# Kernel tuning notes

Measured on AMD Instinct MI355X. Metric: run time of the kernel, lower is better.

## Reference

```python
import jax, jax.numpy as jnp
import numpy as np

N_QUESTION = 10000
B, S = 256, 500
Q_DIM = 128
QA_DIM = 128
M = 64            # memory_size
KEY_DIM = 128
VAL_DIM = 256


def setup_inputs() -> dict:
    key = jax.random.key(0)
    ks = jax.random.split(key, 10)
    q_data = jax.random.randint(ks[0], (B, S), 0, N_QUESTION + 1)
    qa_data = jax.random.randint(ks[1], (B, S), 0, 2 * N_QUESTION + 1)
    # embedding tables with padding_idx=0 zeroed
    q_embed_w = jax.random.normal(ks[2], (N_QUESTION + 1, Q_DIM), jnp.float32) * 0.05
    q_embed_w = q_embed_w.at[0].set(0.0)
    qa_embed_w = jax.random.normal(ks[3], (2 * N_QUESTION + 1, QA_DIM), jnp.float32) * 0.05
    qa_embed_w = qa_embed_w.at[0].set(0.0)
    key_mem = jax.random.normal(ks[4], (M, KEY_DIM), jnp.float32) * (2.0 / KEY_DIM) ** 0.5
    init_value_mem = jax.random.normal(ks[5], (M, VAL_DIM), jnp.float32) * (2.0 / VAL_DIM) ** 0.5
    erase_W = jax.random.normal(ks[6], (QA_DIM, VAL_DIM), jnp.float32) * (2.0 / QA_DIM) ** 0.5
    erase_b = jnp.zeros((VAL_DIM,), jnp.float32)
    add_W = jax.random.normal(ks[7], (QA_DIM, VAL_DIM), jnp.float32) * (2.0 / QA_DIM) ** 0.5
    add_b = jnp.zeros((VAL_DIM,), jnp.float32)
    return {
        "q_data": q_data, "qa_data": qa_data,
        "q_embed_w": q_embed_w, "qa_embed_w": qa_embed_w,
        "key_mem": key_mem, "init_value_mem": init_value_mem,
        "erase_W": erase_W, "erase_b": erase_b,
        "add_W": add_W, "add_b": add_b,
    }


def reference(q_data, qa_data, q_embed_w, qa_embed_w, key_mem, init_value_mem,
              erase_W, erase_b, add_W, add_b):
    q_emb = q_embed_w[q_data]     # [B,S,Qd]
    qa_emb = qa_embed_w[qa_data]  # [B,S,QAd]
    write_mask = (q_data >= 1).astype(jnp.float32)  # [B,S]

    Mv0 = jnp.broadcast_to(init_value_mem[None], (q_data.shape[0], M, VAL_DIM))

    def step(Mv, xs):
        q_t, qa_t, m_t = xs  # [B,Qd], [B,QAd], [B]
        # attention over memory slots
        w = jax.nn.softmax(q_t @ key_mem.T, axis=-1)           # [B,M]
        read = jnp.einsum('bm,bmd->bd', w, Mv)                 # [B,D]
        erase = jax.nn.sigmoid(qa_t @ erase_W + erase_b)       # [B,D]
        add = jnp.tanh(qa_t @ add_W + add_b)                   # [B,D]
        new_Mv = Mv * (1.0 - w[:, :, None] * erase[:, None, :]) \
                 + w[:, :, None] * add[:, None, :]
        Mv = jnp.where(m_t[:, None, None] > 0, new_Mv, Mv)
        return Mv, read

    xs = (jnp.swapaxes(q_emb, 0, 1), jnp.swapaxes(qa_emb, 0, 1),
          jnp.swapaxes(write_mask, 0, 1))
    _, reads = jax.lax.scan(step, Mv0, xs)        # reads: [S,B,D]
    reads = jnp.swapaxes(reads, 0, 1)             # [B,S,D]
    # shift right by one timestep, zero-pad first step
    out = jnp.concatenate([jnp.zeros_like(reads[:, :1]), reads[:, :-1]], axis=1)
    return out
```

## Files before the change

### kernel.cpp

```cpp
#include <hip/hip_runtime.h>
#include <math.h>

#define B_     256
#define S_     500
#define QD_    128
#define M_     64
#define VD_    256
#define CH_    16
#define NQ_    10000
#define NQA_   20000
#define WROWS  (NQ_ + 1)
#define EAROWS (NQA_ + 1)

typedef unsigned int u32;

__device__ __forceinline__ void gload_lds16(const float* g, float* l)
{
    __builtin_amdgcn_global_load_lds(
        (const __attribute__((address_space(1))) u32*)(const void*)g,
        (__attribute__((address_space(3))) u32*)(void*)l, 16, 0, 0);
}

__device__ __forceinline__ float qadd1(float x)
{
    int r = __builtin_amdgcn_mov_dpp(__float_as_int(x), 0xB1, 0xF, 0xF, true);
    return x + __int_as_float(r);
}
__device__ __forceinline__ float qadd2(float x)
{
    int r = __builtin_amdgcn_mov_dpp(__float_as_int(x), 0x4E, 0xF, 0xF, true);
    return x + __int_as_float(r);
}

__global__ void kT_kernel(const float* __restrict__ key_mem, float4* __restrict__ kTq)
{
    int i = blockIdx.x * 256 + threadIdx.x;
    if (i < 32 * 64) {
        int m  = i & 63;
        int k4 = i >> 6;
        kTq[i] = *reinterpret_cast<const float4*>(&key_mem[m * QD_ + k4 * 4]);
    }
}

__global__ __launch_bounds__(256) void wtab_kernel(
    const float*  __restrict__ q_embed_w,
    const float4* __restrict__ kTq,
    float*        __restrict__ wtab)
{
    __shared__ float4 q4[16][32];

    const int tid = threadIdx.x;
    const int r0  = blockIdx.x * 16;

    for (int i = tid; i < 512; i += 256) {
        int row = i >> 5, k4 = i & 31;
        int r   = r0 + row; if (r > NQ_) r = NQ_;
        q4[row][k4] = *reinterpret_cast<const float4*>(
            &q_embed_w[(size_t)r * QD_ + k4 * 4]);
    }
    __syncthreads();

    const int wave = tid >> 6, lane = tid & 63;
    const int rr = wave * 4;

    float s0 = 0.f, s1 = 0.f, s2 = 0.f, s3 = 0.f;
    for (int k4 = 0; k4 < 32; ++k4) {
        float4 kv = kTq[k4 * 64 + lane];
        float4 a0 = q4[rr + 0][k4];
        float4 a1 = q4[rr + 1][k4];
        float4 a2 = q4[rr + 2][k4];
        float4 a3 = q4[rr + 3][k4];
        s0 = fmaf(a0.x, kv.x, s0); s0 = fmaf(a0.y, kv.y, s0);
        s0 = fmaf(a0.z, kv.z, s0); s0 = fmaf(a0.w, kv.w, s0);
        s1 = fmaf(a1.x, kv.x, s1); s1 = fmaf(a1.y, kv.y, s1);
        s1 = fmaf(a1.z, kv.z, s1); s1 = fmaf(a1.w, kv.w, s1);
        s2 = fmaf(a2.x, kv.x, s2); s2 = fmaf(a2.y, kv.y, s2);
        s2 = fmaf(a2.z, kv.z, s2); s2 = fmaf(a2.w, kv.w, s2);
        s3 = fmaf(a3.x, kv.x, s3); s3 = fmaf(a3.y, kv.y, s3);
        s3 = fmaf(a3.z, kv.z, s3); s3 = fmaf(a3.w, kv.w, s3);
    }

    float s[4] = { s0, s1, s2, s3 };
    #pragma unroll
    for (int j = 0; j < 4; ++j) {
        float mx = s[j];
        #pragma unroll
        for (int off = 32; off; off >>= 1) mx = fmaxf(mx, __shfl_xor(mx, off));
        float e = __expf(s[j] - mx);
        float sum = e;
        #pragma unroll
        for (int off = 32; off; off >>= 1) sum += __shfl_xor(sum, off);
        if (r0 + rr + j < WROWS)
            wtab[(size_t)(r0 + rr + j) * 64 + lane] = e / sum;
    }
}

__global__ __launch_bounds__(512) void eatab_kernel(
    const float* __restrict__ qa_embed_w,
    const float* __restrict__ erase_W,
    const float* __restrict__ erase_b,
    const float* __restrict__ add_W,
    const float* __restrict__ add_b,
    float*       __restrict__ eatab)
{
    __shared__ float4 qa4[16][32];

    const int tid = threadIdx.x;
    const int r0  = blockIdx.x * 16;

    {
        int row = tid >> 5, k4 = tid & 31;
        int r   = r0 + row; if (r > NQA_) r = NQA_;
        qa4[row][k4] = *reinterpret_cast<const float4*>(
            &qa_embed_w[(size_t)r * QD_ + k4 * 4]);
    }
    __syncthreads();

    const int  c   = tid & 255;
    const bool isE = tid < 256;
    const float* Wp = isE ? erase_W : add_W;

    float acc[16];
    #pragma unroll
    for (int r = 0; r < 16; ++r) acc[r] = 0.f;

    for (int k4 = 0; k4 < 32; ++k4) {
        float w0 = Wp[(size_t)(k4 * 4 + 0) * 256 + c];
        float w1 = Wp[(size_t)(k4 * 4 + 1) * 256 + c];
        float w2 = Wp[(size_t)(k4 * 4 + 2) * 256 + c];
        float w3 = Wp[(size_t)(k4 * 4 + 3) * 256 + c];
        #pragma unroll
        for (int r = 0; r < 16; ++r) {
            float4 qv = qa4[r][k4];
            acc[r] = fmaf(qv.x, w0, acc[r]);
            acc[r] = fmaf(qv.y, w1, acc[r]);
            acc[r] = fmaf(qv.z, w2, acc[r]);
            acc[r] = fmaf(qv.w, w3, acc[r]);
        }
    }

    const float bias = isE ? erase_b[c] : add_b[c];
    #pragma unroll
    for (int r = 0; r < 16; ++r) {
        float x = acc[r] + bias;
        float y;
        if (isE) {
            y = 1.f / (1.f + __expf(-x));
        } else {
            float t  = __expf(-2.f * fabsf(x));
            float ta = (1.f - t) / (1.f + t);
            y = (x < 0.f) ? -ta : ta;
        }
        if (r0 + r < EAROWS)
            eatab[(size_t)(r0 + r) * 512 + tid] = y;
    }
}

__device__ __forceinline__ void stage_chunk(
    int tb, int tid,
    const int* __restrict__ qrow, const int* __restrict__ qarow,
    const float* __restrict__ wtab, const float* __restrict__ eatab,
    float* wbuf, float* ebuf, float* abuf)
{
    if (tid < 256) {
        int st = tb + (tid >> 4); if (st >= S_) st = S_ - 1;
        gload_lds16(&wtab[(size_t)qrow[st] * 64 + (tid & 15) * 4],
                    &wbuf[(tid & ~63) * 4]);
    }
    #pragma unroll
    for (int j = 0; j < 2; ++j) {
        const int idx = tid + 512 * j;
        int st = tb + (idx >> 6); if (st >= S_) st = S_ - 1;
        const int cq = (idx & 63) * 4;
        const float* rowp = &eatab[(size_t)qarow[st] * 512];
        gload_lds16(&rowp[cq],       &ebuf[(idx & ~63) * 4]);
        gload_lds16(&rowp[256 + cq], &abuf[(idx & ~63) * 4]);
    }
}

__global__ __launch_bounds__(512, 1) void scan_kernel(
    const int*   __restrict__ q_data,
    const int*   __restrict__ qa_data,
    const float* __restrict__ init_mv,
    const float* __restrict__ wtab,
    const float* __restrict__ eatab,
    float*       __restrict__ out)
{
    __shared__ float w_lds[2][CH_ * 64];
    __shared__ float e_lds[2][CH_ * VD_];
    __shared__ float a_lds[2][CH_ * VD_];
    __shared__ int   qrow[S_];
    __shared__ int   qarow[S_];

    const int b   = blockIdx.x;
    const int tid = threadIdx.x;
    const int col = (tid >> 2) * 2;
    const int ms  = tid & 3;
    const int mo  = ms * 16;

    for (int i = tid; i < S_; i += 512) {
        qrow[i]  = q_data[b * S_ + i];
        qarow[i] = qa_data[b * S_ + i];
    }
    __syncthreads();

    stage_chunk(0, tid, qrow, qarow, wtab, eatab,
                w_lds[0], e_lds[0], a_lds[0]);

    float4 mv0[4], mv1[4];
    #pragma unroll
    for (int q = 0; q < 4; ++q) {
        float2 i0 = *reinterpret_cast<const float2*>(&init_mv[(mo + q * 4 + 0) * VD_ + col]);
        float2 i1 = *reinterpret_cast<const float2*>(&init_mv[(mo + q * 4 + 1) * VD_ + col]);
        float2 i2 = *reinterpret_cast<const float2*>(&init_mv[(mo + q * 4 + 2) * VD_ + col]);
        float2 i3 = *reinterpret_cast<const float2*>(&init_mv[(mo + q * 4 + 3) * VD_ + col]);
        mv0[q].x = i0.x; mv1[q].x = i0.y;
        mv0[q].y = i1.x; mv1[q].y = i1.y;
        mv0[q].z = i2.x; mv1[q].z = i2.y;
        mv0[q].w = i3.x; mv1[q].w = i3.y;
    }
    if (ms == 0)
        *reinterpret_cast<float2*>(&out[(size_t)b * S_ * VD_ + col]) = make_float2(0.f, 0.f);

    __syncthreads();

    const int nch = (S_ + CH_ - 1) / CH_;
    for (int c = 0; c < nch; ++c) {
        const int  tb   = c * CH_;
        const int  full = (S_ - tb >= CH_);
        const int  buf  = c & 1;
        const bool hn   = (c + 1 < nch);

        if (hn)
            stage_chunk(tb + CH_, tid, qrow, qarow, wtab, eatab,
                        w_lds[buf ^ 1], e_lds[buf ^ 1], a_lds[buf ^ 1]);

        const float* wb = &w_lds[buf][mo];
        const float* eb = &e_lds[buf][col];
        const float* ab = &a_lds[buf][col];
        float* outp = &out[((size_t)b * S_ + tb + 1) * VD_ + col];

        float4 w0A, w1A, w2A, w3A, w0B, w1B, w2B, w3B;
        float2 evA, avA, evB, avB;
        int    qrA, qrB;

        #define LOADS(tt, SS)                                                   \
            w0##SS = *reinterpret_cast<const float4*>(wb + (tt) * 64 + 0);      \
            w1##SS = *reinterpret_cast<const float4*>(wb + (tt) * 64 + 4);      \
            w2##SS = *reinterpret_cast<const float4*>(wb + (tt) * 64 + 8);      \
            w3##SS = *reinterpret_cast<const float4*>(wb + (tt) * 64 + 12);     \
            ev##SS = *reinterpret_cast<const float2*>(eb + (tt) * VD_);         \
            av##SS = *reinterpret_cast<const float2*>(ab + (tt) * VD_);         \
            qr##SS = qrow[tb + (tt)];

        #define QCORE(WQ, q) {                                                  \
            float4 v0 = mv0[q]; float4 v1 = mv1[q];                             \
            r0a = fmaf(WQ.x, v0.x, r0a); r0b = fmaf(WQ.y, v0.y, r0b);           \
            r0a = fmaf(WQ.z, v0.z, r0a); r0b = fmaf(WQ.w, v0.w, r0b);           \
            r1a = fmaf(WQ.x, v1.x, r1a); r1b = fmaf(WQ.y, v1.y, r1b);           \
            r1a = fmaf(WQ.z, v1.z, r1a); r1b = fmaf(WQ.w, v1.w, r1b);           \
            mv0[q].x = fmaf(WQ.x, fmaf(-em0, v0.x, am0), v0.x);                 \
            mv0[q].y = fmaf(WQ.y, fmaf(-em0, v0.y, am0), v0.y);                 \
            mv0[q].z = fmaf(WQ.z, fmaf(-em0, v0.z, am0), v0.z);                 \
            mv0[q].w = fmaf(WQ.w, fmaf(-em0, v0.w, am0), v0.w);                 \
            mv1[q].x = fmaf(WQ.x, fmaf(-em1, v1.x, am1), v1.x);                 \
            mv1[q].y = fmaf(WQ.y, fmaf(-em1, v1.y, am1), v1.y);                 \
            mv1[q].z = fmaf(WQ.z, fmaf(-em1, v1.z, am1), v1.z);                 \
            mv1[q].w = fmaf(WQ.w, fmaf(-em1, v1.w, am1), v1.w);                 \
        }

        #define COMP(tt, SS, GUARD) {                                           \
            const bool wr  = qr##SS >= 1;                                       \
            const float em0 = wr ? ev##SS.x : 0.f;                              \
            const float am0 = wr ? av##SS.x : 0.f;                              \
            const float em1 = wr ? ev##SS.y : 0.f;                              \
            const float am1 = wr ? av##SS.y : 0.f;                              \
            float r0a = 0.f, r0b = 0.f, r1a = 0.f, r1b = 0.f;                   \
            QCORE(w0##SS, 0) QCORE(w1##SS, 1) QCORE(w2##SS, 2) QCORE(w3##SS, 3) \
            float rd0 = qadd2(qadd1(r0a + r0b));                                \
            float rd1 = qadd2(qadd1(r1a + r1b));                                \
            if (ms == 0 && (GUARD))                                             \
                *reinterpret_cast<float2*>(&outp[(size_t)(tt) * VD_]) =         \
                    make_float2(rd0, rd1);                                      \
        }

        if (full) {
            LOADS(0, A)
            LOADS(1,  B) COMP(0,  A, true)
            LOADS(2,  A) COMP(1,  B, true)
            LOADS(3,  B) COMP(2,  A, true)
            LOADS(4,  A) COMP(3,  B, true)
            LOADS(5,  B) COMP(4,  A, true)
            LOADS(6,  A) COMP(5,  B, true)
            LOADS(7,  B) COMP(6,  A, true)
            LOADS(8,  A) COMP(7,  B, true)
            LOADS(9,  B) COMP(8,  A, true)
            LOADS(10, A) COMP(9,  B, true)
            LOADS(11, B) COMP(10, A, true)
            LOADS(12, A) COMP(11, B, true)
            LOADS(13, B) COMP(12, A, true)
            LOADS(14, A) COMP(13, B, true)
            LOADS(15, B) COMP(14, A, true)
            COMP(15, B, true)
        } else {
            #define TSTEP(tt)                                                   \
            if (tb + (tt) < S_) {                                               \
                LOADS(tt, A)                                                    \
                COMP(tt, A, tb + (tt) + 1 < S_)                                 \
            }
            TSTEP(0)  TSTEP(1)  TSTEP(2)  TSTEP(3)
            TSTEP(4)  TSTEP(5)  TSTEP(6)  TSTEP(7)
            TSTEP(8)  TSTEP(9)  TSTEP(10) TSTEP(11)
            TSTEP(12) TSTEP(13) TSTEP(14) TSTEP(15)
            #undef TSTEP
        }

        #undef COMP
        #undef QCORE
        #undef LOADS

        __syncthreads();
    }
}

extern "C" void kernel_launch(void* const* d_in, const int* in_sizes, int n_in,
                              void* d_out, int out_size, void* d_ws, size_t ws_size,
                              hipStream_t stream)
{
    const int*   q_data  = (const int*)  d_in[0];
    const int*   qa_data = (const int*)  d_in[1];
    const float* q_emb   = (const float*)d_in[2];
    const float* qa_emb  = (const float*)d_in[3];
    const float* key_mem = (const float*)d_in[4];
    const float* init_mv = (const float*)d_in[5];
    const float* erase_W = (const float*)d_in[6];
    const float* erase_b = (const float*)d_in[7];
    const float* add_W   = (const float*)d_in[8];
    const float* add_b   = (const float*)d_in[9];
    float* out = (float*)d_out;

    char* ws = (char*)d_ws;
    float4* kTq = (float4*)ws;
    size_t off = (size_t)2048 * sizeof(float4);
    float* wtab = (float*)(ws + off);
    off += (size_t)WROWS * 64 * sizeof(float);
    off = (off + 255) & ~(size_t)255;
    float* eatab = (float*)(ws + off);
    off += (size_t)EAROWS * 512 * sizeof(float);

    kT_kernel<<<dim3(8), dim3(256), 0, stream>>>(key_mem, kTq);
    wtab_kernel<<<dim3((WROWS + 15) / 16), dim3(256), 0, stream>>>(
        q_emb, kTq, wtab);
    eatab_kernel<<<dim3((EAROWS + 15) / 16), dim3(512), 0, stream>>>(
        qa_emb, erase_W, erase_b, add_W, add_b, eatab);
    scan_kernel<<<dim3(B_), dim3(512), 0, stream>>>(
        q_data, qa_data, init_mv, wtab, eatab, out);
}
```

Before: 313.2 us.

## Split scan across two column-half blocks per batch with interleaved erase/add table

Launches two blocks per batch row, each owning half of the value columns, so the serial scan runs on 512 blocks with 8 memory slots per thread instead of 16. The erase and add tables are interleaved per column so one float4 LDS load supplies both erase and add for two columns, and the slot reduction uses an extra row-mirror DPP step across 8 lanes. Launch bounds now allow several blocks per CU, which reduces register budget and can cause spills; the q-side attention weights are staged redundantly by both blocks.

```diff
diff --git a/kernel.cpp b/kernel.cpp
--- a/kernel.cpp
+++ b/kernel.cpp
@@ -29,6 +29,11 @@
 __device__ __forceinline__ float qadd2(float x)
 {
     int r = __builtin_amdgcn_mov_dpp(__float_as_int(x), 0x4E, 0xF, 0xF, true);
+    return x + __int_as_float(r);
+}
+__device__ __forceinline__ float qaddm(float x)
+{
+    int r = __builtin_amdgcn_mov_dpp(__float_as_int(x), 0x141, 0xF, 0xF, true);
     return x + __int_as_float(r);
 }
 
@@ -152,15 +157,15 @@
             y = (x < 0.f) ? -ta : ta;
         }
         if (r0 + r < EAROWS)
-            eatab[(size_t)(r0 + r) * 512 + tid] = y;
+            eatab[(size_t)(r0 + r) * 512 + c * 2 + (isE ? 0 : 1)] = y;
     }
 }
 
 __device__ __forceinline__ void stage_chunk(
-    int tb, int tid,
+    int tb, int tid, int cb,
     const int* __restrict__ qrow, const int* __restrict__ qarow,
     const float* __restrict__ wtab, const float* __restrict__ eatab,
-    float* wbuf, float* ebuf, float* abuf)
+    float* wbuf, float* eabuf)
 {
     if (tid < 256) {
         int st = tb + (tid >> 4); if (st >= S_) st = S_ - 1;
@@ -172,13 +177,12 @@
         const int idx = tid + 512 * j;
         int st = tb + (idx >> 6); if (st >= S_) st = S_ - 1;
         const int cq = (idx & 63) * 4;
-        const float* rowp = &eatab[(size_t)qarow[st] * 512];
-        gload_lds16(&rowp[cq],       &ebuf[(idx & ~63) * 4]);
-        gload_lds16(&rowp[256 + cq], &abuf[(idx & ~63) * 4]);
-    }
-}
-
-__global__ __launch_bounds__(512, 1) void scan_kernel(
+        gload_lds16(&eatab[(size_t)qarow[st] * 512 + cb * 256 + cq],
+                    &eabuf[(idx & ~63) * 4]);
+    }
+}
+
+__global__ __launch_bounds__(512, 4) void scan_kernel(
     const int*   __restrict__ q_data,
     const int*   __restrict__ qa_data,
     const float* __restrict__ init_mv,
@@ -187,16 +191,18 @@
     float*       __restrict__ out)
 {
     __shared__ float w_lds[2][CH_ * 64];
-    __shared__ float e_lds[2][CH_ * VD_];
-    __shared__ float a_lds[2][CH_ * VD_];
+    __shared__ float ea_lds[2][CH_ * 256];
     __shared__ int   qrow[S_];
     __shared__ int   qarow[S_];
 
-    const int b   = blockIdx.x;
-    const int tid = threadIdx.x;
-    const int col = (tid >> 2) * 2;
-    const int ms  = tid & 3;
-    const int mo  = ms * 16;
+    const int bid  = blockIdx.x;
+    const int b    = bid >> 1;
+    const int cb   = bid & 1;
+    const int tid  = threadIdx.x;
+    const int mgrp = tid & 7;
+    const int colg = tid >> 3;
+    const int mo   = mgrp * 8;
+    const int col  = cb * 128 + colg * 2;
 
     for (int i = tid; i < S_; i += 512) {
         qrow[i]  = q_data[b * S_ + i];
@@ -204,22 +210,16 @@
     }
     __syncthreads();
 
-    stage_chunk(0, tid, qrow, qarow, wtab, eatab,
-                w_lds[0], e_lds[0], a_lds[0]);
-
-    float4 mv0[4], mv1[4];
-    #pragma unroll
-    for (int q = 0; q < 4; ++q) {
-        float2 i0 = *reinterpret_cast<const float2*>(&init_mv[(mo + q * 4 + 0) * VD_ + col]);
-        float2 i1 = *reinterpret_cast<const float2*>(&init_mv[(mo + q * 4 + 1) * VD_ + col]);
-        float2 i2 = *reinterpret_cast<const float2*>(&init_mv[(mo + q * 4 + 2) * VD_ + col]);
-        float2 i3 = *reinterpret_cast<const float2*>(&init_mv[(mo + q * 4 + 3) * VD_ + col]);
-        mv0[q].x = i0.x; mv1[q].x = i0.y;
-        mv0[q].y = i1.x; mv1[q].y = i1.y;
-        mv0[q].z = i2.x; mv1[q].z = i2.y;
-        mv0[q].w = i3.x; mv1[q].w = i3.y;
-    }
-    if (ms == 0)
+    stage_chunk(0, tid, cb, qrow, qarow, wtab, eatab, w_lds[0], ea_lds[0]);
+
+    float mv0[8], mv1[8];
+    #pragma unroll
+    for (int k = 0; k < 8; ++k) {
+        float2 iv = *reinterpret_cast<const float2*>(&init_mv[(mo + k) * VD_ + col]);
+        mv0[k] = iv.x;
+        mv1[k] = iv.y;
+    }
+    if (mgrp == 0)
         *reinterpret_cast<float2*>(&out[(size_t)b * S_ * VD_ + col]) = make_float2(0.f, 0.f);
 
     __syncthreads();
@@ -232,54 +232,42 @@
         const bool hn   = (c + 1 < nch);
 
         if (hn)
-            stage_chunk(tb + CH_, tid, qrow, qarow, wtab, eatab,
-                        w_lds[buf ^ 1], e_lds[buf ^ 1], a_lds[buf ^ 1]);
+            stage_chunk(tb + CH_, tid, cb, qrow, qarow, wtab, eatab,
+                        w_lds[buf ^ 1], ea_lds[buf ^ 1]);
 
         const float* wb = &w_lds[buf][mo];
-        const float* eb = &e_lds[buf][col];
-        const float* ab = &a_lds[buf][col];
+        const float* eb = &ea_lds[buf][colg * 4];
         float* outp = &out[((size_t)b * S_ + tb + 1) * VD_ + col];
 
-        float4 w0A, w1A, w2A, w3A, w0B, w1B, w2B, w3B;
-        float2 evA, avA, evB, avB;
+        float4 wq0A, wq1A, wq0B, wq1B, eaA, eaB;
         int    qrA, qrB;
 
         #define LOADS(tt, SS)                                                   \
-            w0##SS = *reinterpret_cast<const float4*>(wb + (tt) * 64 + 0);      \
-            w1##SS = *reinterpret_cast<const float4*>(wb + (tt) * 64 + 4);      \
-            w2##SS = *reinterpret_cast<const float4*>(wb + (tt) * 64 + 8);      \
-            w3##SS = *reinterpret_cast<const float4*>(wb + (tt) * 64 + 12);     \
-            ev##SS = *reinterpret_cast<const float2*>(eb + (tt) * VD_);         \
-            av##SS = *reinterpret_cast<const float2*>(ab + (tt) * VD_);         \
-            qr##SS = qrow[tb + (tt)];
-
-        #define QCORE(WQ, q) {                                                  \
-            float4 v0 = mv0[q]; float4 v1 = mv1[q];                             \
-            r0a = fmaf(WQ.x, v0.x, r0a); r0b = fmaf(WQ.y, v0.y, r0b);           \
-            r0a = fmaf(WQ.z, v0.z, r0a); r0b = fmaf(WQ.w, v0.w, r0b);           \
-            r1a = fmaf(WQ.x, v1.x, r1a); r1b = fmaf(WQ.y, v1.y, r1b);           \
-            r1a = fmaf(WQ.z, v1.z, r1a); r1b = fmaf(WQ.w, v1.w, r1b);           \
-            mv0[q].x = fmaf(WQ.x, fmaf(-em0, v0.x, am0), v0.x);                 \
-            mv0[q].y = fmaf(WQ.y, fmaf(-em0, v0.y, am0), v0.y);                 \
-            mv0[q].z = fmaf(WQ.z, fmaf(-em0, v0.z, am0), v0.z);                 \
-            mv0[q].w = fmaf(WQ.w, fmaf(-em0, v0.w, am0), v0.w);                 \
-            mv1[q].x = fmaf(WQ.x, fmaf(-em1, v1.x, am1), v1.x);                 \
-            mv1[q].y = fmaf(WQ.y, fmaf(-em1, v1.y, am1), v1.y);                 \
-            mv1[q].z = fmaf(WQ.z, fmaf(-em1, v1.z, am1), v1.z);                 \
-            mv1[q].w = fmaf(WQ.w, fmaf(-em1, v1.w, am1), v1.w);                 \
+            wq0##SS = *reinterpret_cast<const float4*>(wb + (tt) * 64);         \
+            wq1##SS = *reinterpret_cast<const float4*>(wb + (tt) * 64 + 4);     \
+            ea##SS  = *reinterpret_cast<const float4*>(eb + (tt) * 256);        \
+            qr##SS  = qrow[tb + (tt)];
+
+        #define QE(W, K) {                                                      \
+            const float v0 = mv0[K], v1 = mv1[K];                               \
+            r0 = fmaf(W, v0, r0);                                               \
+            r1 = fmaf(W, v1, r1);                                               \
+            mv0[K] = fmaf(W, fmaf(-em0, v0, am0), v0);                          \
+            mv1[K] = fmaf(W, fmaf(-em1, v1, am1), v1);                          \
         }
 
         #define COMP(tt, SS, GUARD) {                                           \
-            const bool wr  = qr##SS >= 1;                                       \
-            const float em0 = wr ? ev##SS.x : 0.f;                              \
-            const float am0 = wr ? av##SS.x : 0.f;                              \
-            const float em1 = wr ? ev##SS.y : 0.f;                              \
-            const float am1 = wr ? av##SS.y : 0.f;                              \
-            float r0a = 0.f, r0b = 0.f, r1a = 0.f, r1b = 0.f;                   \
-            QCORE(w0##SS, 0) QCORE(w1##SS, 1) QCORE(w2##SS, 2) QCORE(w3##SS, 3) \
-            float rd0 = qadd2(qadd1(r0a + r0b));                                \
-            float rd1 = qadd2(qadd1(r1a + r1b));                                \
-            if (ms == 0 && (GUARD))                                             \
+            const bool  wr  = qr##SS >= 1;                                      \
+            const float em0 = wr ? ea##SS.x : 0.f;                              \
+            const float am0 = wr ? ea##SS.y : 0.f;                              \
+            const float em1 = wr ? ea##SS.z : 0.f;                              \
+            const float am1 = wr ? ea##SS.w : 0.f;                              \
+            float r0 = 0.f, r1 = 0.f;                                           \
+            QE(wq0##SS.x, 0) QE(wq0##SS.y, 1) QE(wq0##SS.z, 2) QE(wq0##SS.w, 3) \
+            QE(wq1##SS.x, 4) QE(wq1##SS.y, 5) QE(wq1##SS.z, 6) QE(wq1##SS.w, 7) \
+            float rd0 = qaddm(qadd2(qadd1(r0)));                                \
+            float rd1 = qaddm(qadd2(qadd1(r1)));                                \
+            if (mgrp == 0 && (GUARD))                                           \
                 *reinterpret_cast<float2*>(&outp[(size_t)(tt) * VD_]) =         \
                     make_float2(rd0, rd1);                                      \
         }
@@ -316,7 +304,7 @@
         }
 
         #undef COMP
-        #undef QCORE
+        #undef QE
         #undef LOADS
 
         __syncthreads();
@@ -353,6 +341,6 @@
         q_emb, kTq, wtab);
     eatab_kernel<<<dim3((EAROWS + 15) / 16), dim3(512), 0, stream>>>(
         qa_emb, erase_W, erase_b, add_W, add_b, eatab);
-    scan_kernel<<<dim3(B_), dim3(512), 0, stream>>>(
+    scan_kernel<<<dim3(B_ * 2), dim3(512), 0, stream>>>(
         q_data, qa_data, init_mv, wtab, eatab, out);
 }
```

Result: slower. 321.0 us (+2.5%).
